# Optimization experiments

Hardware: AMD Instinct MI355X
Metric: run time of the kernel (lower is better)

Reference implementation:

```python
import jax, jax.numpy as jnp
import numpy as np

S = 14
C = 20
STEP = 1.0 / 14
LAMBDA_COORD = 5.0
LAMBDA_NOOBJ = 0.5
EPS = 1e-7


def setup_inputs() -> dict:
    key = jax.random.key(0)
    k1, k2 = jax.random.split(key)
    pred = jax.random.uniform(k1, (4096, S, S, 10 + C), dtype=jnp.float32)
    target = jax.random.uniform(k2, (4096, S, S, 10 + C), dtype=jnp.float32)
    return {"pred": pred, "target": target}


def _convert_cell_box(box, ix, jy):
    # box: [..., 2, 4] in (cell-rel cx, cell-rel cy, w, h); returns clamped (x1, y1, w, h)
    x = (box[..., 0] + ix) * STEP - box[..., 2] / 2
    y = (box[..., 1] + jy) * STEP - box[..., 3] / 2
    out = jnp.stack([x, y, box[..., 2], box[..., 3]], axis=-1)
    return jnp.clip(out, 0.0)


def _paired_iou(b1, b2):
    # b1, b2: [..., 4] as (x, y, w, h)
    x1, y1, w1, h1 = b1[..., 0], b1[..., 1], b1[..., 2], b1[..., 3]
    x2, y2, w2, h2 = b2[..., 0], b2[..., 1], b2[..., 2], b2[..., 3]
    inter_w = w1 + w2 - (jnp.maximum(x1 + w1, x2 + w2) - jnp.minimum(x1, x2))
    inter_h = h1 + h2 - (jnp.maximum(y1 + h1, y2 + h2) - jnp.minimum(y1, y2))
    inter = jnp.clip(inter_w, 0.0) * jnp.clip(inter_h, 0.0)
    union = w1 * h1 + w2 * h2 - inter + EPS
    return inter / union


def _xywh_to_xyxy(box):
    cx, cy, w, h = box[..., 0], box[..., 1], box[..., 2], box[..., 3]
    return jnp.stack([cx - w / 2, cy - h / 2, cx + w / 2, cy + h / 2], axis=-1)


def _bbox_iou_xyxy(b1, b2):
    x1 = jnp.maximum(b1[..., 0], b2[..., 0])
    y1 = jnp.maximum(b1[..., 1], b2[..., 1])
    x2 = jnp.minimum(b1[..., 2], b2[..., 2])
    y2 = jnp.minimum(b1[..., 3], b2[..., 3])
    inter = jnp.clip(x2 - x1, 0.0) * jnp.clip(y2 - y1, 0.0)
    a1 = jnp.clip(b1[..., 2] - b1[..., 0], 0.0) * jnp.clip(b1[..., 3] - b1[..., 1], 0.0)
    a2 = jnp.clip(b2[..., 2] - b2[..., 0], 0.0) * jnp.clip(b2[..., 3] - b2[..., 1], 0.0)
    return inter / (a1 + a2 - inter + EPS)


def _yolo_loss(pred, target):
    N = pred.shape[0]
    dt = pred.dtype
    pb = pred[..., :10].reshape(N, S, S, 2, 5)
    tb = target[..., :10].reshape(N, S, S, 2, 5)
    pcls = pred[..., 10:]
    tcls = target[..., 10:]

    obj_mask = tb[..., 4] > 0          # [N,S,S,2]
    sig_mask = obj_mask[..., 1]        # [N,S,S]

    # grid offsets: dim1 is y (j), dim2 is x (i)
    ix = jnp.arange(S, dtype=dt)[None, None, :, None]
    jy = jnp.arange(S, dtype=dt)[None, :, None, None]
    p_conv = _convert_cell_box(pb[..., :4], ix, jy)
    t_conv = _convert_cell_box(tb[..., :4], ix, jy)
    ious = _paired_iou(p_conv, t_conv)          # [N,S,S,2]
    max_i = jnp.argmax(ious, axis=-1)           # [N,S,S]

    # where sig_mask: zero out the non-argmax anchor of obj_mask
    keep = (~sig_mask[..., None]) | (jnp.arange(2)[None, None, None, :] == max_i[..., None])
    obj_mask = obj_mask & keep

    fm = obj_mask.astype(dt)
    dconf2 = (pb[..., 4] - tb[..., 4]) ** 2
    obj_loss = jnp.sum(fm * dconf2)
    noobj_loss = jnp.sum((1.0 - fm) * dconf2)

    # Alpha-DIoU (alpha=0.5) over obj cells
    pxy = _xywh_to_xyxy(pb[..., :4])
    txy = _xywh_to_xyxy(tb[..., :4])
    iou = jnp.maximum(_bbox_iou_xyxy(pxy, txy), EPS)
    pcx = (pxy[..., 0] + pxy[..., 2]) / 2
    pcy = (pxy[..., 1] + pxy[..., 3]) / 2
    tcx = (txy[..., 0] + txy[..., 2]) / 2
    tcy = (txy[..., 1] + txy[..., 3]) / 2
    center_dist = (pcx - tcx) ** 2 + (pcy - tcy) ** 2
    ex1 = jnp.minimum(pxy[..., 0], txy[..., 0])
    ey1 = jnp.minimum(pxy[..., 1], txy[..., 1])
    ex2 = jnp.maximum(pxy[..., 2], txy[..., 2])
    ey2 = jnp.maximum(pxy[..., 3], txy[..., 3])
    diag = (ex2 - ex1) ** 2 + (ey2 - ey1) ** 2 + EPS
    diou_per = (1.0 - jnp.sqrt(iou)) + center_dist / diag
    n_obj = jnp.sum(fm)
    bbox_loss = jnp.where(n_obj > 0, jnp.sum(fm * diou_per) / jnp.maximum(n_obj, 1.0), 0.0)

    # Focal-MSE class loss over sig cells
    sm = sig_mask.astype(dt)
    ce = (pcls - tcls) ** 2
    pt = jnp.clip(jnp.exp(-ce), EPS, 1.0)
    focal = (1.0 - pt) ** 2 * ce
    n_cls = jnp.sum(sm) * C
    class_loss = jnp.where(n_cls > 0, jnp.sum(sm[..., None] * focal) / jnp.maximum(n_cls, 1.0), 0.0)

    total = obj_loss + LAMBDA_NOOBJ * noobj_loss + LAMBDA_COORD * bbox_loss + class_loss
    return total / N


def reference(pred, target):
    return _yolo_loss(pred, target)
```

## Files before the change

kernel.cpp:

```cpp
#include <hip/hip_runtime.h>
#include <math.h>


#define SGRID 14
#define NCLS 20
#define F4_PER_TILE 480
#define NT_TILES 12544

constexpr float STEPF  = 1.0f / 14.0f;
constexpr float EPSF   = 1e-7f;
constexpr float L_COORD = 5.0f;
constexpr float L_NOOBJ = 0.5f;

__device__ __forceinline__ float waveSum(float v) {
#pragma unroll
    for (int o = 32; o > 0; o >>= 1) v += __shfl_down(v, o);
    return v;
}

__device__ __forceinline__ void gload_lds16(const float4* gsrc, float4* ldst) {
    __builtin_amdgcn_global_load_lds(
        (const __attribute__((address_space(1))) void*)gsrc,
        (__attribute__((address_space(3))) void*)ldst, 16, 0, 0);
}

__device__ __forceinline__ void issueTile(const float4* pred4, const float4* targ4,
                                          int tile, int l, float4* dst) {
    const float4* psrc = pred4 + (size_t)tile * F4_PER_TILE;
    const float4* tsrc = targ4 + (size_t)tile * F4_PER_TILE;
#pragma unroll
    for (int i = 0; i < 15; ++i) {
        int g = i * 64 + l;
        const float4* src = (g < F4_PER_TILE) ? (psrc + g) : (tsrc + (g - F4_PER_TILE));
        gload_lds16(src, dst + i * 64);
    }
}

__global__ __launch_bounds__(128) void yolo_main(const float* __restrict__ pred,
                                                 const float* __restrict__ targ,
                                                 float* __restrict__ ws) {
    __shared__ float4 stage[2][2][2 * F4_PER_TILE];
    __shared__ float red[2][6];

    const int t = threadIdx.x;
    const int w = t >> 6;
    const int l = t & 63;

    float s[6] = {0.f, 0.f, 0.f, 0.f, 0.f, 0.f};

    const int G = gridDim.x * 2;
    const int gwave = blockIdx.x * 2 + w;

    const float4* pred4 = reinterpret_cast<const float4*>(pred);
    const float4* targ4 = reinterpret_cast<const float4*>(targ);

    int buf = 0;
    if (gwave < NT_TILES) issueTile(pred4, targ4, gwave, l, stage[w][0]);

    for (int tile = gwave; tile < NT_TILES; tile += G) {
        const int nxt = tile + G;

        if (nxt < NT_TILES) {
            asm volatile("s_waitcnt lgkmcnt(0)" ::: "memory");
            __builtin_amdgcn_sched_barrier(0);
            issueTile(pred4, targ4, nxt, l, stage[w][buf ^ 1]);
            asm volatile("s_waitcnt vmcnt(15)" ::: "memory");
        } else {
            asm volatile("s_waitcnt vmcnt(0)" ::: "memory");
        }
        __builtin_amdgcn_sched_barrier(0);

        const float4* wbuf = stage[w][buf];
        buf ^= 1;

        float pv[30], tv[30];
        {
            const float2* cp = reinterpret_cast<const float2*>(wbuf) + l * 15;
            const float2* ct = reinterpret_cast<const float2*>(wbuf + F4_PER_TILE) + l * 15;
#pragma unroll
            for (int j = 0; j < 15; ++j) {
                float2 a = cp[j]; pv[2 * j] = a.x; pv[2 * j + 1] = a.y;
                float2 b = ct[j]; tv[2 * j] = b.x; tv[2 * j + 1] = b.y;
            }
        }

        const float* p = pv;
        const float* tt = tv;
        int cell = tile * 64 + l;
        float ix = (float)(cell % SGRID);
        float jy = (float)((cell / SGRID) % SGRID);

        float iouP[2];
#pragma unroll
        for (int b = 0; b < 2; ++b) {
            const float* pb = p + 5 * b;
            const float* tb = tt + 5 * b;
            float px = fmaxf((pb[0] + ix) * STEPF - pb[2] * 0.5f, 0.f);
            float py = fmaxf((pb[1] + jy) * STEPF - pb[3] * 0.5f, 0.f);
            float pw = fmaxf(pb[2], 0.f), ph = fmaxf(pb[3], 0.f);
            float tx = fmaxf((tb[0] + ix) * STEPF - tb[2] * 0.5f, 0.f);
            float ty = fmaxf((tb[1] + jy) * STEPF - tb[3] * 0.5f, 0.f);
            float tw = fmaxf(tb[2], 0.f), th = fmaxf(tb[3], 0.f);
            float iw = pw + tw - (fmaxf(px + pw, tx + tw) - fminf(px, tx));
            float ih = ph + th - (fmaxf(py + ph, ty + th) - fminf(py, ty));
            float inter = fmaxf(iw, 0.f) * fmaxf(ih, 0.f);
            float uni = pw * ph + tw * th - inter + EPSF;
            iouP[b] = inter / uni;
        }
        int maxi = (iouP[1] > iouP[0]) ? 1 : 0;
        bool sig = tt[9] > 0.f;

#pragma unroll
        for (int b = 0; b < 2; ++b) {
            const float* pb = p + 5 * b;
            const float* tb = tt + 5 * b;
            bool om = tb[4] > 0.f;
            bool kp = (!sig) || (b == maxi);
            float f = (om && kp) ? 1.f : 0.f;

            float d = pb[4] - tb[4];
            float d2 = d * d;
            s[0] += f * d2;
            s[1] += (1.f - f) * d2;

            float px1 = pb[0] - pb[2] * 0.5f, py1 = pb[1] - pb[3] * 0.5f;
            float px2 = pb[0] + pb[2] * 0.5f, py2 = pb[1] + pb[3] * 0.5f;
            float tx1 = tb[0] - tb[2] * 0.5f, ty1 = tb[1] - tb[3] * 0.5f;
            float tx2 = tb[0] + tb[2] * 0.5f, ty2 = tb[1] + tb[3] * 0.5f;

            float xi1 = fmaxf(px1, tx1), yi1 = fmaxf(py1, ty1);
            float xi2 = fminf(px2, tx2), yi2 = fminf(py2, ty2);
            float inter = fmaxf(xi2 - xi1, 0.f) * fmaxf(yi2 - yi1, 0.f);
            float a1 = fmaxf(px2 - px1, 0.f) * fmaxf(py2 - py1, 0.f);
            float a2 = fmaxf(tx2 - tx1, 0.f) * fmaxf(ty2 - ty1, 0.f);
            float iou = fmaxf(inter / (a1 + a2 - inter + EPSF), EPSF);

            float pcx = (px1 + px2) * 0.5f, pcy = (py1 + py2) * 0.5f;
            float tcx = (tx1 + tx2) * 0.5f, tcy = (ty1 + ty2) * 0.5f;
            float cd = (pcx - tcx) * (pcx - tcx) + (pcy - tcy) * (pcy - tcy);
            float ex1 = fminf(px1, tx1), ey1 = fminf(py1, ty1);
            float ex2 = fmaxf(px2, tx2), ey2 = fmaxf(py2, ty2);
            float diag = (ex2 - ex1) * (ex2 - ex1) + (ey2 - ey1) * (ey2 - ey1) + EPSF;
            float diou = 1.f - sqrtf(iou) + cd / diag;

            s[2] += f * diou;
            s[3] += f;
        }

        float fs = 0.f;
#pragma unroll
        for (int k = 0; k < NCLS; ++k) {
            float ce = p[10 + k] - tt[10 + k];
            ce *= ce;
            float pt = __expf(-ce);
            pt = fminf(fmaxf(pt, EPSF), 1.0f);
            float om1 = 1.f - pt;
            fs += om1 * om1 * ce;
        }
        float smv = sig ? 1.f : 0.f;
        s[4] += smv * fs;
        s[5] += smv;
    }

#pragma unroll
    for (int q = 0; q < 6; ++q) s[q] = waveSum(s[q]);
    if (l == 0) {
#pragma unroll
        for (int q = 0; q < 6; ++q) red[w][q] = s[q];
    }
    __syncthreads();
    if (t == 0) {
        float v[6];
#pragma unroll
        for (int q = 0; q < 6; ++q) v[q] = red[0][q] + red[1][q];
        float4* o = reinterpret_cast<float4*>(ws + (size_t)blockIdx.x * 8);
        o[0] = make_float4(v[0], v[1], v[2], v[3]);
        o[1] = make_float4(v[4], v[5], 0.f, 0.f);
    }
}

__global__ __launch_bounds__(256) void yolo_reduce(const float* __restrict__ ws,
                                                   float* __restrict__ out,
                                                   int nBlocks, float invN) {
    float s[6] = {0.f, 0.f, 0.f, 0.f, 0.f, 0.f};
    for (int row = threadIdx.x; row < nBlocks; row += 256) {
        const float4* r4 = reinterpret_cast<const float4*>(ws + (size_t)row * 8);
        float4 a = r4[0], b = r4[1];
        s[0] += a.x; s[1] += a.y; s[2] += a.z; s[3] += a.w; s[4] += b.x; s[5] += b.y;
    }
#pragma unroll
    for (int q = 0; q < 6; ++q) s[q] = waveSum(s[q]);

    __shared__ float red[4][6];
    int lane = threadIdx.x & 63;
    int wv   = threadIdx.x >> 6;
    if (lane == 0) {
#pragma unroll
        for (int q = 0; q < 6; ++q) red[wv][q] = s[q];
    }
    __syncthreads();
    if (threadIdx.x == 0) {
        float obj   = red[0][0] + red[1][0] + red[2][0] + red[3][0];
        float noobj = red[0][1] + red[1][1] + red[2][1] + red[3][1];
        float bboxS = red[0][2] + red[1][2] + red[2][2] + red[3][2];
        float nObj  = red[0][3] + red[1][3] + red[2][3] + red[3][3];
        float clsS  = red[0][4] + red[1][4] + red[2][4] + red[3][4];
        float smS   = red[0][5] + red[1][5] + red[2][5] + red[3][5];

        float bbox_loss = (nObj > 0.f) ? (bboxS / fmaxf(nObj, 1.f)) : 0.f;
        float nCls = smS * (float)NCLS;
        float class_loss = (nCls > 0.f) ? (clsS / fmaxf(nCls, 1.f)) : 0.f;
        float total = obj + L_NOOBJ * noobj + L_COORD * bbox_loss + class_loss;
        out[0] = total * invN;
    }
}

extern "C" void kernel_launch(void* const* d_in, const int* in_sizes, int n_in,
                              void* d_out, int out_size, void* d_ws, size_t ws_size,
                              hipStream_t stream) {
    const float* pred = (const float*)d_in[0];
    const float* targ = (const float*)d_in[1];
    float* out = (float*)d_out;
    float* ws = (float*)d_ws;

    int N = in_sizes[0] / (SGRID * SGRID * 30);
    (void)N;
    int blocks = 512;

    yolo_main<<<blocks, 128, 0, stream>>>(pred, targ, ws);
    yolo_reduce<<<1, 256, 0, stream>>>(ws, out, blocks, 1.0f / 4096.0f);
}
```

Before: 39.12 us.

## Split each cell across two lanes and use 4-wave blocks with smaller tiles

Each wave now handles 32 cells per tile instead of 64, and each pair of lanes shares one cell: each lane takes one of the two boxes and half of the 20 class terms, exchanging the IoU via a lane shuffle. Tiles are halved, so the per-lane register arrays go away and the tail of the target data is fetched with 4-byte global-to-LDS loads. Blocks grow to 256 threads with launch bounds set to 2 blocks per CU. The aim is to cut register pressure, raise occupancy and spread the per-cell work more evenly, at the cost of more tile iterations, extra shuffles and smaller load batches per wave.

```diff
diff --git a/kernel.cpp b/kernel.cpp
--- a/kernel.cpp
+++ b/kernel.cpp
@@ -4,8 +4,10 @@
 
 #define SGRID 14
 #define NCLS 20
-#define F4_PER_TILE 480
-#define NT_TILES 12544
+#define CELLS_PER_TILE 32
+#define F4_PER_INPUT 240
+#define TILE_F4 480
+#define NT_TILES 25088
 
 constexpr float STEPF  = 1.0f / 14.0f;
 constexpr float EPSF   = 1e-7f;
@@ -18,38 +20,51 @@
     return v;
 }
 
-__device__ __forceinline__ void gload_lds16(const float4* gsrc, float4* ldst) {
+__device__ __forceinline__ void gload_lds16(const void* gsrc, void* ldst) {
     __builtin_amdgcn_global_load_lds(
         (const __attribute__((address_space(1))) void*)gsrc,
         (__attribute__((address_space(3))) void*)ldst, 16, 0, 0);
 }
+__device__ __forceinline__ void gload_lds4(const void* gsrc, void* ldst) {
+    __builtin_amdgcn_global_load_lds(
+        (const __attribute__((address_space(1))) void*)gsrc,
+        (__attribute__((address_space(3))) void*)ldst, 4, 0, 0);
+}
 
 __device__ __forceinline__ void issueTile(const float4* pred4, const float4* targ4,
                                           int tile, int l, float4* dst) {
-    const float4* psrc = pred4 + (size_t)tile * F4_PER_TILE;
-    const float4* tsrc = targ4 + (size_t)tile * F4_PER_TILE;
-#pragma unroll
-    for (int i = 0; i < 15; ++i) {
+    const float4* psrc = pred4 + (size_t)tile * F4_PER_INPUT;
+    const float4* tsrc = targ4 + (size_t)tile * F4_PER_INPUT;
+#pragma unroll
+    for (int i = 0; i < 7; ++i) {
         int g = i * 64 + l;
-        const float4* src = (g < F4_PER_TILE) ? (psrc + g) : (tsrc + (g - F4_PER_TILE));
+        const float4* src = (g < F4_PER_INPUT) ? (psrc + g) : (tsrc + (g - F4_PER_INPUT));
         gload_lds16(src, dst + i * 64);
     }
-}
-
-__global__ __launch_bounds__(128) void yolo_main(const float* __restrict__ pred,
-                                                 const float* __restrict__ targ,
-                                                 float* __restrict__ ws) {
-    __shared__ float4 stage[2][2][2 * F4_PER_TILE];
-    __shared__ float red[2][6];
+    const float* tf = reinterpret_cast<const float*>(tsrc);
+    float* df = reinterpret_cast<float*>(dst);
+#pragma unroll
+    for (int j = 0; j < 2; ++j) {
+        gload_lds4(tf + 832 + j * 64 + l, df + 1792 + j * 64);
+    }
+}
+
+__global__ __launch_bounds__(256, 2) void yolo_main(const float* __restrict__ pred,
+                                                    const float* __restrict__ targ,
+                                                    float* __restrict__ ws) {
+    __shared__ float4 stage[4][2][TILE_F4];
+    __shared__ float red[4][6];
 
     const int t = threadIdx.x;
     const int w = t >> 6;
     const int l = t & 63;
-
-    float s[6] = {0.f, 0.f, 0.f, 0.f, 0.f, 0.f};
-
-    const int G = gridDim.x * 2;
-    const int gwave = blockIdx.x * 2 + w;
+    const int c = l >> 1;
+    const int b = l & 1;
+
+    float s0 = 0.f, s1 = 0.f, s2 = 0.f, s3 = 0.f, s4 = 0.f, s5 = 0.f;
+
+    const int G = gridDim.x * 4;
+    const int gwave = blockIdx.x * 4 + w;
 
     const float4* pred4 = reinterpret_cast<const float4*>(pred);
     const float4* targ4 = reinterpret_cast<const float4*>(targ);
@@ -59,109 +74,110 @@
 
     for (int tile = gwave; tile < NT_TILES; tile += G) {
         const int nxt = tile + G;
-
         if (nxt < NT_TILES) {
             asm volatile("s_waitcnt lgkmcnt(0)" ::: "memory");
             __builtin_amdgcn_sched_barrier(0);
             issueTile(pred4, targ4, nxt, l, stage[w][buf ^ 1]);
-            asm volatile("s_waitcnt vmcnt(15)" ::: "memory");
+            asm volatile("s_waitcnt vmcnt(9)" ::: "memory");
         } else {
             asm volatile("s_waitcnt vmcnt(0)" ::: "memory");
         }
         __builtin_amdgcn_sched_barrier(0);
 
-        const float4* wbuf = stage[w][buf];
+        const float* P = reinterpret_cast<const float*>(stage[w][buf]);
+        const float* T = P + 960;
         buf ^= 1;
 
-        float pv[30], tv[30];
-        {
-            const float2* cp = reinterpret_cast<const float2*>(wbuf) + l * 15;
-            const float2* ct = reinterpret_cast<const float2*>(wbuf + F4_PER_TILE) + l * 15;
-#pragma unroll
-            for (int j = 0; j < 15; ++j) {
-                float2 a = cp[j]; pv[2 * j] = a.x; pv[2 * j + 1] = a.y;
-                float2 b = ct[j]; tv[2 * j] = b.x; tv[2 * j + 1] = b.y;
-            }
-        }
-
-        const float* p = pv;
-        const float* tt = tv;
-        int cell = tile * 64 + l;
+        const float2* p2 = reinterpret_cast<const float2*>(P + 30 * c);
+        const float2* t2 = reinterpret_cast<const float2*>(T + 30 * c);
+        float2 pA = p2[2 * b], pB = p2[2 * b + 1], pC = p2[2 * b + 2];
+        float2 tA = t2[2 * b], tB = t2[2 * b + 1], tC = t2[2 * b + 2];
+        float t9v = (T + 30 * c)[9];
+        float p0 = b ? pA.y : pA.x;
+        float p1 = b ? pB.x : pA.y;
+        float p2f = b ? pB.y : pB.x;
+        float p3f = b ? pC.x : pB.y;
+        float p4f = b ? pC.y : pC.x;
+        float t0 = b ? tA.y : tA.x;
+        float t1 = b ? tB.x : tA.y;
+        float t2f = b ? tB.y : tB.x;
+        float t3f = b ? tC.x : tB.y;
+        float t4f = b ? tC.y : tC.x;
+
+        int cell = tile * CELLS_PER_TILE + c;
         float ix = (float)(cell % SGRID);
         float jy = (float)((cell / SGRID) % SGRID);
 
-        float iouP[2];
-#pragma unroll
-        for (int b = 0; b < 2; ++b) {
-            const float* pb = p + 5 * b;
-            const float* tb = tt + 5 * b;
-            float px = fmaxf((pb[0] + ix) * STEPF - pb[2] * 0.5f, 0.f);
-            float py = fmaxf((pb[1] + jy) * STEPF - pb[3] * 0.5f, 0.f);
-            float pw = fmaxf(pb[2], 0.f), ph = fmaxf(pb[3], 0.f);
-            float tx = fmaxf((tb[0] + ix) * STEPF - tb[2] * 0.5f, 0.f);
-            float ty = fmaxf((tb[1] + jy) * STEPF - tb[3] * 0.5f, 0.f);
-            float tw = fmaxf(tb[2], 0.f), th = fmaxf(tb[3], 0.f);
-            float iw = pw + tw - (fmaxf(px + pw, tx + tw) - fminf(px, tx));
-            float ih = ph + th - (fmaxf(py + ph, ty + th) - fminf(py, ty));
-            float inter = fmaxf(iw, 0.f) * fmaxf(ih, 0.f);
-            float uni = pw * ph + tw * th - inter + EPSF;
-            iouP[b] = inter / uni;
+        float px = fmaxf((p0 + ix) * STEPF - p2f * 0.5f, 0.f);
+        float py = fmaxf((p1 + jy) * STEPF - p3f * 0.5f, 0.f);
+        float pw = fmaxf(p2f, 0.f), ph = fmaxf(p3f, 0.f);
+        float tx = fmaxf((t0 + ix) * STEPF - t2f * 0.5f, 0.f);
+        float ty = fmaxf((t1 + jy) * STEPF - t3f * 0.5f, 0.f);
+        float tw = fmaxf(t2f, 0.f), th = fmaxf(t3f, 0.f);
+        float iw = pw + tw - (fmaxf(px + pw, tx + tw) - fminf(px, tx));
+        float ih = ph + th - (fmaxf(py + ph, ty + th) - fminf(py, ty));
+        float inter0 = fmaxf(iw, 0.f) * fmaxf(ih, 0.f);
+        float iouP = inter0 / (pw * ph + tw * th - inter0 + EPSF);
+
+        float other = __shfl_xor(iouP, 1);
+        float i0 = b ? other : iouP;
+        float i1 = b ? iouP : other;
+        int maxi = (i1 > i0) ? 1 : 0;
+        bool sig = t9v > 0.f;
+        bool om = t4f > 0.f;
+        bool kp = (!sig) || (b == maxi);
+        float f = (om && kp) ? 1.f : 0.f;
+
+        float d = p4f - t4f;
+        float d2 = d * d;
+        s0 += f * d2;
+        s1 += (1.f - f) * d2;
+
+        float px1 = p0 - p2f * 0.5f, py1 = p1 - p3f * 0.5f;
+        float px2 = p0 + p2f * 0.5f, py2 = p1 + p3f * 0.5f;
+        float tx1 = t0 - t2f * 0.5f, ty1 = t1 - t3f * 0.5f;
+        float tx2 = t0 + t2f * 0.5f, ty2 = t1 + t3f * 0.5f;
+
+        float xi1 = fmaxf(px1, tx1), yi1 = fmaxf(py1, ty1);
+        float xi2 = fminf(px2, tx2), yi2 = fminf(py2, ty2);
+        float inter = fmaxf(xi2 - xi1, 0.f) * fmaxf(yi2 - yi1, 0.f);
+        float a1 = fmaxf(px2 - px1, 0.f) * fmaxf(py2 - py1, 0.f);
+        float a2 = fmaxf(tx2 - tx1, 0.f) * fmaxf(ty2 - ty1, 0.f);
+        float iou = fmaxf(inter / (a1 + a2 - inter + EPSF), EPSF);
+
+        float pcx = (px1 + px2) * 0.5f, pcy = (py1 + py2) * 0.5f;
+        float tcx = (tx1 + tx2) * 0.5f, tcy = (ty1 + ty2) * 0.5f;
+        float cd = (pcx - tcx) * (pcx - tcx) + (pcy - tcy) * (pcy - tcy);
+        float ex1 = fminf(px1, tx1), ey1 = fminf(py1, ty1);
+        float ex2 = fmaxf(px2, tx2), ey2 = fmaxf(py2, ty2);
+        float diag = (ex2 - ex1) * (ex2 - ex1) + (ey2 - ey1) * (ey2 - ey1) + EPSF;
+        float diou = 1.f - sqrtf(iou) + cd / diag;
+
+        s2 += f * diou;
+        s3 += f;
+
+        const float2* pc2 = reinterpret_cast<const float2*>(P + 30 * c + 10 + 10 * b);
+        const float2* tc2 = reinterpret_cast<const float2*>(T + 30 * c + 10 + 10 * b);
+        float fs = 0.f;
+#pragma unroll
+        for (int m = 0; m < 5; ++m) {
+            float2 a = pc2[m], e = tc2[m];
+            float ce1 = a.x - e.x; ce1 *= ce1;
+            float pt1 = fminf(fmaxf(__expf(-ce1), EPSF), 1.0f);
+            float o1 = 1.f - pt1;
+            fs += o1 * o1 * ce1;
+            float ce2 = a.y - e.y; ce2 *= ce2;
+            float pt2 = fminf(fmaxf(__expf(-ce2), EPSF), 1.0f);
+            float o2 = 1.f - pt2;
+            fs += o2 * o2 * ce2;
         }
-        int maxi = (iouP[1] > iouP[0]) ? 1 : 0;
-        bool sig = tt[9] > 0.f;
-
-#pragma unroll
-        for (int b = 0; b < 2; ++b) {
-            const float* pb = p + 5 * b;
-            const float* tb = tt + 5 * b;
-            bool om = tb[4] > 0.f;
-            bool kp = (!sig) || (b == maxi);
-            float f = (om && kp) ? 1.f : 0.f;
-
-            float d = pb[4] - tb[4];
-            float d2 = d * d;
-            s[0] += f * d2;
-            s[1] += (1.f - f) * d2;
-
-            float px1 = pb[0] - pb[2] * 0.5f, py1 = pb[1] - pb[3] * 0.5f;
-            float px2 = pb[0] + pb[2] * 0.5f, py2 = pb[1] + pb[3] * 0.5f;
-            float tx1 = tb[0] - tb[2] * 0.5f, ty1 = tb[1] - tb[3] * 0.5f;
-            float tx2 = tb[0] + tb[2] * 0.5f, ty2 = tb[1] + tb[3] * 0.5f;
-
-            float xi1 = fmaxf(px1, tx1), yi1 = fmaxf(py1, ty1);
-            float xi2 = fminf(px2, tx2), yi2 = fminf(py2, ty2);
-            float inter = fmaxf(xi2 - xi1, 0.f) * fmaxf(yi2 - yi1, 0.f);
-            float a1 = fmaxf(px2 - px1, 0.f) * fmaxf(py2 - py1, 0.f);
-            float a2 = fmaxf(tx2 - tx1, 0.f) * fmaxf(ty2 - ty1, 0.f);
-            float iou = fmaxf(inter / (a1 + a2 - inter + EPSF), EPSF);
-
-            float pcx = (px1 + px2) * 0.5f, pcy = (py1 + py2) * 0.5f;
-            float tcx = (tx1 + tx2) * 0.5f, tcy = (ty1 + ty2) * 0.5f;
-            float cd = (pcx - tcx) * (pcx - tcx) + (pcy - tcy) * (pcy - tcy);
-            float ex1 = fminf(px1, tx1), ey1 = fminf(py1, ty1);
-            float ex2 = fmaxf(px2, tx2), ey2 = fmaxf(py2, ty2);
-            float diag = (ex2 - ex1) * (ex2 - ex1) + (ey2 - ey1) * (ey2 - ey1) + EPSF;
-            float diou = 1.f - sqrtf(iou) + cd / diag;
-
-            s[2] += f * diou;
-            s[3] += f;
+        if (sig) {
+            s4 += fs;
+            if (b == 0) s5 += 1.f;
         }
-
-        float fs = 0.f;
-#pragma unroll
-        for (int k = 0; k < NCLS; ++k) {
-            float ce = p[10 + k] - tt[10 + k];
-            ce *= ce;
-            float pt = __expf(-ce);
-            pt = fminf(fmaxf(pt, EPSF), 1.0f);
-            float om1 = 1.f - pt;
-            fs += om1 * om1 * ce;
-        }
-        float smv = sig ? 1.f : 0.f;
-        s[4] += smv * fs;
-        s[5] += smv;
-    }
-
+    }
+
+    float s[6] = { s0, s1, s2, s3, s4, s5 };
 #pragma unroll
     for (int q = 0; q < 6; ++q) s[q] = waveSum(s[q]);
     if (l == 0) {
@@ -172,7 +188,7 @@
     if (t == 0) {
         float v[6];
 #pragma unroll
-        for (int q = 0; q < 6; ++q) v[q] = red[0][q] + red[1][q];
+        for (int q = 0; q < 6; ++q) v[q] = red[0][q] + red[1][q] + red[2][q] + red[3][q];
         float4* o = reinterpret_cast<float4*>(ws + (size_t)blockIdx.x * 8);
         o[0] = make_float4(v[0], v[1], v[2], v[3]);
         o[1] = make_float4(v[4], v[5], 0.f, 0.f);
@@ -185,8 +201,8 @@
     float s[6] = {0.f, 0.f, 0.f, 0.f, 0.f, 0.f};
     for (int row = threadIdx.x; row < nBlocks; row += 256) {
         const float4* r4 = reinterpret_cast<const float4*>(ws + (size_t)row * 8);
-        float4 a = r4[0], b = r4[1];
-        s[0] += a.x; s[1] += a.y; s[2] += a.z; s[3] += a.w; s[4] += b.x; s[5] += b.y;
+        float4 a = r4[0], bq = r4[1];
+        s[0] += a.x; s[1] += a.y; s[2] += a.z; s[3] += a.w; s[4] += bq.x; s[5] += bq.y;
     }
 #pragma unroll
     for (int q = 0; q < 6; ++q) s[q] = waveSum(s[q]);
@@ -223,10 +239,8 @@
     float* out = (float*)d_out;
     float* ws = (float*)d_ws;
 
-    int N = in_sizes[0] / (SGRID * SGRID * 30);
-    (void)N;
     int blocks = 512;
 
-    yolo_main<<<blocks, 128, 0, stream>>>(pred, targ, ws);
+    yolo_main<<<blocks, 256, 0, stream>>>(pred, targ, ws);
     yolo_reduce<<<1, 256, 0, stream>>>(ws, out, blocks, 1.0f / 4096.0f);
 }
```

New measurement: 37.94 us, median of 2. -3.0%, faster.
